# Kernel optimization log

Measured on AMD Instinct MI355X. Metric: run time of the kernel, lower is better.

## Reference

```python
import jax, jax.numpy as jnp
import numpy as np

# PGA G(3,0,1), basis order [1, e0,e1,e2,e3, e01,e02,e03,e12,e13,e23, e012,e013,e023,e123, e0123].
# Non-degenerate blades (no e0 factor) kept by the inner-product mask:
INNER_COORDS = jnp.array([0, 2, 3, 4, 8, 9, 10, 14])

B, S, C_IN, MV = 4, 2048, 3, 16
HID, NH, BLADES = 32, 8, 9


def setup_inputs() -> dict:
    key = jax.random.key(0)
    ks = jax.random.split(key, 8)
    return {
        "x": jax.random.normal(ks[0], (B, S, C_IN, MV), dtype=jnp.float32),
        "blade": jax.random.normal(ks[1], (BLADES, MV, MV), dtype=jnp.float32) * 0.3,
        "w_enter": jax.random.uniform(ks[2], (HID, C_IN, BLADES), dtype=jnp.float32),
        "w_q": jax.random.uniform(ks[3], (HID * NH, HID, BLADES), dtype=jnp.float32),
        "w_k": jax.random.uniform(ks[4], (HID, HID, BLADES), dtype=jnp.float32),
        "w_v": jax.random.uniform(ks[5], (HID, HID, BLADES), dtype=jnp.float32),
        "w_out": jax.random.uniform(ks[6], (HID, HID * NH, BLADES), dtype=jnp.float32),
        "w_final": jax.random.uniform(ks[7], (HID, HID, BLADES), dtype=jnp.float32),
    }


def equi_linear(w, blade, x):
    # torch: einsum('j i b, b x y, ... i x -> ... j y'); fuse blade into weight first.
    wb = jnp.einsum("jib,bxy->jixy", w, blade)  # [out, in, 16, 16]
    return jnp.einsum("jixy,bsix->bsjy", wb, x)


def equi_norm(x):
    ip = jnp.sum(jnp.take(x, INNER_COORDS, axis=-1) ** 2, axis=-1, keepdims=True)
    sq = jnp.mean(ip, axis=-2, keepdims=True)  # mean over mv channels
    return x / jnp.sqrt(sq)


def geometric_attention(hn, blade, w_q, w_k, w_v, w_out):
    b, s = hn.shape[0], hn.shape[1]
    q = equi_linear(w_q, blade, hn)  # [b, s, HID*NH, 16]
    k = equi_linear(w_k, blade, hn)  # [b, s, HID, 16]
    v = equi_linear(w_v, blade, hn)
    # rearrange '... items (hidden n_heads) mv -> ... n_heads items hidden mv'
    q = q.reshape(b, s, HID, NH, MV).transpose(0, 3, 1, 2, 4)  # [b, nh, s, HID, 16]
    qs = jnp.take(q, INNER_COORDS, axis=-1).reshape(b, NH, s, HID * 8)
    ks = jnp.take(k, INNER_COORDS, axis=-1).reshape(b, s, HID * 8)  # shared head (dim 1)
    vs = v.reshape(b, s, HID * MV)
    scale = 1.0 / jnp.sqrt(jnp.asarray(HID * 8, dtype=qs.dtype))
    scores = jnp.einsum("bhsd,btd->bhst", qs, ks) * scale  # [b, nh, s, s]
    attn = jax.nn.softmax(scores, axis=-1)
    out = jnp.einsum("bhst,btd->bhsd", attn, vs)  # [b, nh, s, HID*16]
    out = out[..., : HID * MV].reshape(b, NH, s, HID, MV)
    # '... heads items hidden x -> ... items (heads hidden) x'
    out = out.transpose(0, 2, 1, 3, 4).reshape(b, s, NH * HID, MV)
    return equi_linear(w_out, blade, out)  # [b, s, HID, 16]


def reference(x, blade, w_enter, w_q, w_k, w_v, w_out, w_final):
    h = equi_linear(w_enter, blade, x)  # initial projection -> [b, s, HID, 16]
    res = h
    hn = equi_norm(h)  # attention_equinorm
    a = geometric_attention(hn, blade, w_q, w_k, w_v, w_out)
    h = res + a  # residual around attention block
    return equi_linear(w_final, blade, h)  # final output projection
```

## Files before the change

kernel.cpp:

```cpp
#include <hip/hip_runtime.h>


typedef unsigned short u16;
typedef unsigned int u32;
typedef __attribute__((ext_vector_type(4))) float f32x4;
typedef __attribute__((ext_vector_type(8))) _Float16 half8;

__device__ inline u16 f2h(float f) {
  _Float16 h = (_Float16)f;
  return __builtin_bit_cast(u16, h);
}
__device__ inline float h2f(u16 u) { return (float)__builtin_bit_cast(_Float16, u); }

__device__ inline void async_cp16(const void* g, void* l) {
  __builtin_amdgcn_global_load_lds((const __attribute__((address_space(1))) u32*)g,
                                   (__attribute__((address_space(3))) u32*)l, 16, 0, 0);
}

__device__ inline f32x4 mfma16(half8 a, half8 b, f32x4 c) {
  return __builtin_amdgcn_mfma_f32_16x16x32_f16(a, b, c, 0, 0, 0);
}

template <int CTRL>
__device__ inline float dpp_mv(float v) {
  int i = __builtin_bit_cast(int, v);
  return __builtin_bit_cast(float, __builtin_amdgcn_update_dpp(i, i, CTRL, 0xf, 0xf, false));
}

#define IC_PACK 0xEA984320u

#define Q_LD 4096

__global__ void build_wb_enter(const float* __restrict__ we, const float* __restrict__ blade,
                               float* __restrict__ out) {
  int idx = blockIdx.x * 256 + threadIdx.x;
  if (idx >= 32 * 48 * 16) return;
  int j = idx / 768;
  int rem = idx - j * 768;
  int ix = rem >> 4, y = rem & 15;
  int i = ix >> 4, x = ix & 15;
  float acc = 0.f;
#pragma unroll
  for (int bb = 0; bb < 9; ++bb) acc += we[j * 27 + i * 9 + bb] * blade[bb * 256 + x * 16 + y];
  out[idx] = acc;
}

__global__ void build_wqkvT(const float* __restrict__ wq, const float* __restrict__ wk,
                            const float* __restrict__ wv, const float* __restrict__ blade,
                            u16* __restrict__ out) {
  int idx = blockIdx.x * 256 + threadIdx.x;
  if (idx >= 2816 * 1024) return;
  int k = idx & 1023, n = idx >> 10;
  int kk = k & 511;
  int i = kk >> 4, x = kk & 15;
  const float* w;
  int y;
  float scale = 1.0f;
  if (n < 2048) {
    int j = n >> 3;
    y = (IC_PACK >> ((n & 7) * 4)) & 15;
    w = wq + j * 288 + i * 9;
    scale = 0.09016844005556021f;
  } else if (n < 2304) {
    int m = n - 2048;
    int j = m >> 3;
    y = (IC_PACK >> ((m & 7) * 4)) & 15;
    w = wk + j * 288 + i * 9;
  } else {
    int m = n - 2304;
    int j = m >> 4;
    y = m & 15;
    w = wv + j * 288 + i * 9;
  }
  float acc = 0.f;
#pragma unroll
  for (int bb = 0; bb < 9; ++bb) acc += w[bb] * blade[bb * 256 + x * 16 + y];
  out[idx] = f2h(acc * scale);
}

__global__ void build_woutT(const float* __restrict__ wo, const float* __restrict__ blade,
                            u16* __restrict__ out) {
  int idx = blockIdx.x * 256 + threadIdx.x;
  if (idx >= 512 * 4096) return;
  int k = idx & 4095, n = idx >> 12;
  int j = n >> 4, y = n & 15;
  int c = k >> 4, x = k & 15;
  float acc = 0.f;
#pragma unroll
  for (int bb = 0; bb < 9; ++bb) acc += wo[j * 2304 + c * 9 + bb] * blade[bb * 256 + x * 16 + y];
  out[idx] = f2h(acc);
}

__global__ void build_wfinalT(const float* __restrict__ wf, const float* __restrict__ blade,
                              u16* __restrict__ out) {
  int idx = blockIdx.x * 256 + threadIdx.x;
  if (idx >= 512 * 512) return;
  int k = idx & 511, n = idx >> 9;
  int j = n >> 4, y = n & 15;
  int i = k >> 4, x = k & 15;
  float acc = 0.f;
#pragma unroll
  for (int bb = 0; bb < 9; ++bb) acc += wf[j * 288 + i * 9 + bb] * blade[bb * 256 + x * 16 + y];
  out[idx] = f2h(acc);
}

__global__ __launch_bounds__(256) void enter_norm(const float* __restrict__ x,
                                                  const float* __restrict__ wb,
                                                  float* __restrict__ h, u16* __restrict__ hn) {
  const int tid = threadIdx.x;
  const int tl = tid >> 5, j = tid & 31;
  const int token = blockIdx.x * 8 + tl;
  const float* xp = x + (size_t)token * 48;
  float xv[48];
#pragma unroll
  for (int q = 0; q < 12; ++q) {
    float4 t = ((const float4*)xp)[q];
    xv[q * 4 + 0] = t.x;
    xv[q * 4 + 1] = t.y;
    xv[q * 4 + 2] = t.z;
    xv[q * 4 + 3] = t.w;
  }
  float acc[16] = {};
  const float* wp = wb + j * 768;
#pragma unroll
  for (int t = 0; t < 48; ++t) {
    const float xs = xv[t];
    const float4* w4 = (const float4*)(wp + t * 16);
#pragma unroll
    for (int u = 0; u < 4; ++u) {
      float4 wv = w4[u];
      acc[u * 4 + 0] += xs * wv.x;
      acc[u * 4 + 1] += xs * wv.y;
      acc[u * 4 + 2] += xs * wv.z;
      acc[u * 4 + 3] += xs * wv.w;
    }
  }
  float ip = acc[0] * acc[0] + acc[2] * acc[2] + acc[3] * acc[3] + acc[4] * acc[4] +
             acc[8] * acc[8] + acc[9] * acc[9] + acc[10] * acc[10] + acc[14] * acc[14];
#pragma unroll
  for (int d = 1; d < 32; d <<= 1) ip += __shfl_xor(ip, d, 64);
  const float r = 1.0f / sqrtf(ip * (1.0f / 32.0f));
  float* hp = h + (size_t)token * 512 + j * 16;
#pragma unroll
  for (int u = 0; u < 4; ++u)
    ((float4*)hp)[u] = make_float4(acc[u * 4 + 0], acc[u * 4 + 1], acc[u * 4 + 2], acc[u * 4 + 3]);
  u16 hb[16], lb[16];
#pragma unroll
  for (int y = 0; y < 16; ++y) {
    float sv = acc[y] * r;
    u16 hv = f2h(sv);
    hb[y] = hv;
    lb[y] = f2h(sv - h2f(hv));
  }
  u16* hq = hn + (size_t)token * 1024 + j * 16;
  ((uint4*)hq)[0] = *(const uint4*)&hb[0];
  ((uint4*)hq)[1] = *(const uint4*)&hb[8];
  u16* lq = hq + 512;
  ((uint4*)lq)[0] = *(const uint4*)&lb[0];
  ((uint4*)lq)[1] = *(const uint4*)&lb[8];
}

template <int MODE>
__global__ __launch_bounds__(256) void gemm_bt(const u16* __restrict__ A,
                                               const u16* __restrict__ BT, int M, int N, int K,
                                               u16* __restrict__ Co, float* __restrict__ Cf,
                                               const float* __restrict__ res,
                                               u16* __restrict__ kvp, int ldc) {
  __shared__ u16 ltA[4096];
  __shared__ u16 ltB[4096];
  const int tid = threadIdx.x;
  const int lane = tid & 63;
  const int wid = tid >> 6;
  const int quad = lane >> 4, colc = lane & 15;
  const int m0 = blockIdx.y * 128, n0 = blockIdx.x * 128;
  const int wrow = (wid >> 1) * 64, wcol = (wid & 1) * 64;
  f32x4 acc[4][4] = {};
  const int r0 = tid >> 2;
  const int swk = (((tid & 3) ^ ((tid >> 2) & 3)) << 3);
  const u16* Ab = A + (size_t)(m0 + r0) * K + swk;
  const u16* Ab2 = Ab + (size_t)64 * K;
  const u16* Bb = BT + (size_t)(n0 + r0) * K + swk;
  const u16* Bb2 = Bb + (size_t)64 * K;
  const int swr = ((colc & 3) << 3);
  for (int k0 = 0; k0 < K; k0 += 32) {
    __syncthreads();
    async_cp16(Ab + k0, &ltA[tid * 8]);
    async_cp16(Ab2 + k0, &ltA[2048 + tid * 8]);
    async_cp16(Bb + k0, &ltB[tid * 8]);
    async_cp16(Bb2 + k0, &ltB[2048 + tid * 8]);
    __syncthreads();
    half8 af[4], bfr[4];
#pragma unroll
    for (int i2 = 0; i2 < 4; ++i2)
      af[i2] = *(const half8*)&ltA[(wrow + i2 * 16 + colc) * 32 + ((quad << 3) ^ swr)];
#pragma unroll
    for (int j2 = 0; j2 < 4; ++j2)
      bfr[j2] = *(const half8*)&ltB[(wcol + j2 * 16 + colc) * 32 + ((quad << 3) ^ swr)];
#pragma unroll
    for (int i2 = 0; i2 < 4; ++i2)
#pragma unroll
      for (int j2 = 0; j2 < 4; ++j2) acc[i2][j2] = mfma16(af[i2], bfr[j2], acc[i2][j2]);
  }
#pragma unroll
  for (int i2 = 0; i2 < 4; ++i2) {
#pragma unroll
    for (int j2 = 0; j2 < 4; ++j2) {
      const int mb = m0 + wrow + i2 * 16 + quad * 4;
      const int n = n0 + wcol + j2 * 16 + colc;
      if constexpr (MODE == 0) {
        if (n < 2048) {
#pragma unroll
          for (int rg = 0; rg < 4; ++rg) {
            const int m = mb + rg;
            float v = acc[i2][j2][rg];
            u16 hv = f2h(v);
            Co[(size_t)m * ldc + n] = hv;
            Co[(size_t)m * ldc + 2048 + n] = f2h(v - h2f(hv));
          }
        } else if (n < 2304) {
          const int d = n - 2048;
#pragma unroll
          for (int rg = 0; rg < 4; ++rg) {
            const int m = mb + rg;
            int bb2 = m >> 11, s = m & 2047, t = s >> 5, key = s & 31;
            size_t blk = ((size_t)(bb2 * 64 + t)) << 15;
            int off2 = key * 256 + ((((d >> 3) ^ (key & 7)) << 3)) + (d & 7);
            float v = acc[i2][j2][rg];
            u16 hv = f2h(v);
            kvp[blk + off2] = hv;
            kvp[blk + 8192 + off2] = f2h(v - h2f(hv));
          }
        } else {
          const int vd = n - 2304;
          int bb2 = mb >> 11, s0 = mb & 2047, t = s0 >> 5, key0 = s0 & 31;
          size_t blk = ((size_t)(bb2 * 64 + t)) << 15;
          u16 tmp[4];
#pragma unroll
          for (int rg = 0; rg < 4; ++rg) tmp[rg] = f2h(acc[i2][j2][rg]);
          size_t idx =
              blk + 16384 + vd * 32 + ((((key0 >> 3) ^ ((vd >> 1) & 3)) << 3)) + (key0 & 7);
          *(uint2*)&kvp[idx] = *(const uint2*)tmp;
        }
      } else {
#pragma unroll
        for (int rg = 0; rg < 4; ++rg) {
          const int m = mb + rg;
          float v = acc[i2][j2][rg];
          if constexpr (MODE == 1) {
            v += res[(size_t)m * ldc + n];
            Co[(size_t)m * ldc + n] = f2h(v * (1.0f / 256.0f));
          } else {
            Cf[(size_t)m * ldc + n] = v * 256.0f;
          }
        }
      }
    }
  }
}

__global__ __launch_bounds__(256, 2) void flash_attn(const u16* __restrict__ qbuf,
                                                     const u16* __restrict__ kvp,
                                                     u16* __restrict__ out) {
  __shared__ u16 lds[35600];
  u16* kp = lds;
  u16* lp = lds + 8192;
  u16* vp = lds + 16384;
  u16* pbuf = lds + 32768;
  float* alpha_s = (float*)(lds + 35328);
  float* l_s = (float*)(lds + 35456);
  int* flg = (int*)(lds + 35584);
  const int tid = threadIdx.x, lane = tid & 63, wid = tid >> 6;
  const int quad = lane >> 4, colc = lane & 15;
  const int b = blockIdx.z, h = blockIdx.y, qb = blockIdx.x;
  half8 qh[8], ql[8];
  {
    const u16* qr = qbuf + (size_t)(b * 2048 + qb * 64 + wid * 16 + colc) * Q_LD + h * 8;
#pragma unroll
    for (int kb = 0; kb < 8; ++kb) {
      qh[kb] = *(const half8*)(qr + (kb * 4 + quad) * 64);
      ql[kb] = *(const half8*)(qr + 2048 + (kb * 4 + quad) * 64);
    }
  }
  f32x4 oacc[4][8] = {};
  float mrun[4], lrun[4];
#pragma unroll
  for (int rg = 0; rg < 4; ++rg) {
    mrun[rg] = -1e30f;
    lrun[rg] = 0.f;
  }
  const u16* kvb = kvp + ((size_t)(b * 64) << 15);
  const int x0 = colc & 7;
  for (int it = 0; it < 64; ++it) {
    __syncthreads();
    {
      const u16* src = kvb + ((size_t)it << 15);
#pragma unroll
      for (int c = 0; c < 16; ++c) {
        int e = c * 256 + tid;
        async_cp16(src + e * 8, &lds[e * 8]);
      }
    }
    __syncthreads();
    f32x4 s0a = {}, s0b = {}, s1a = {}, s1b = {};
#pragma unroll
    for (int kb = 0; kb < 8; ++kb) {
      const int sw = (((kb * 4 + quad) ^ x0) << 3);
      half8 khi0 = *(const half8*)&kp[colc * 256 + sw];
      half8 khi1 = *(const half8*)&kp[(16 + colc) * 256 + sw];
      half8 klo0 = *(const half8*)&lp[colc * 256 + sw];
      half8 klo1 = *(const half8*)&lp[(16 + colc) * 256 + sw];
      s0a = mfma16(qh[kb], khi0, s0a);
      s0b = mfma16(ql[kb], khi0, s0b);
      s1a = mfma16(qh[kb], khi1, s1a);
      s1b = mfma16(ql[kb], khi1, s1b);
      if (kb & 1) {
        s0b = mfma16(qh[kb], klo0, s0b);
        s1b = mfma16(qh[kb], klo1, s1b);
      } else {
        s0a = mfma16(qh[kb], klo0, s0a);
        s1a = mfma16(qh[kb], klo1, s1a);
      }
    }
    f32x4 sfr[2];
    sfr[0] = s0a + s0b;
    sfr[1] = s1a + s1b;
    float mx[4];
#pragma unroll
    for (int rg = 0; rg < 4; ++rg) mx[rg] = fmaxf(sfr[0][rg], sfr[1][rg]);
#pragma unroll
    for (int rg = 0; rg < 4; ++rg) mx[rg] = fmaxf(mx[rg], dpp_mv<0x121>(mx[rg]));
#pragma unroll
    for (int rg = 0; rg < 4; ++rg) mx[rg] = fmaxf(mx[rg], dpp_mv<0x122>(mx[rg]));
#pragma unroll
    for (int rg = 0; rg < 4; ++rg) mx[rg] = fmaxf(mx[rg], dpp_mv<0x124>(mx[rg]));
#pragma unroll
    for (int rg = 0; rg < 4; ++rg) mx[rg] = fmaxf(mx[rg], dpp_mv<0x128>(mx[rg]));
    float al[4], pv0[4], pv1[4], rs[4];
#pragma unroll
    for (int rg = 0; rg < 4; ++rg) {
      float mn = fmaxf(mrun[rg], mx[rg]);
      al[rg] = exp2f(mrun[rg] - mn);
      mrun[rg] = mn;
      pv0[rg] = exp2f(sfr[0][rg] - mn);
      pv1[rg] = exp2f(sfr[1][rg] - mn);
      rs[rg] = pv0[rg] + pv1[rg];
    }
#pragma unroll
    for (int rg = 0; rg < 4; ++rg) rs[rg] += dpp_mv<0x121>(rs[rg]);
#pragma unroll
    for (int rg = 0; rg < 4; ++rg) rs[rg] += dpp_mv<0x122>(rs[rg]);
#pragma unroll
    for (int rg = 0; rg < 4; ++rg) rs[rg] += dpp_mv<0x124>(rs[rg]);
#pragma unroll
    for (int rg = 0; rg < 4; ++rg) rs[rg] += dpp_mv<0x128>(rs[rg]);
    const int prow = wid * 16 + quad * 4;
#pragma unroll
    for (int rg = 0; rg < 4; ++rg) {
      lrun[rg] = lrun[rg] * al[rg] + rs[rg];
      pbuf[(prow + rg) * 40 + colc] = f2h(pv0[rg]);
      pbuf[(prow + rg) * 40 + 16 + colc] = f2h(pv1[rg]);
    }
    {
      float nd = __builtin_fabsf(al[0] - 1.f) + __builtin_fabsf(al[1] - 1.f) +
                 __builtin_fabsf(al[2] - 1.f) + __builtin_fabsf(al[3] - 1.f);
      int own = __any(nd != 0.f);
      if (lane == 0) flg[wid] = own;
    }
    if (colc == 0) {
#pragma unroll
      for (int rg = 0; rg < 4; ++rg) alpha_s[prow + rg] = al[rg];
    }
    __syncthreads();
    half8 vf[8];
#pragma unroll
    for (int vb = 0; vb < 8; ++vb) {
      const int vd = wid * 128 + vb * 16 + colc;
      vf[vb] = *(const half8*)&vp[vd * 32 + ((quad ^ ((vd >> 1) & 3)) << 3)];
    }
    half8 pf[4];
#pragma unroll
    for (int pa = 0; pa < 4; ++pa) pf[pa] = *(const half8*)&pbuf[(pa * 16 + colc) * 40 + quad * 8];
    const int need = flg[0] | flg[1] | flg[2] | flg[3];
    if (need) {
      float av[4][4];
#pragma unroll
      for (int pa = 0; pa < 4; ++pa)
#pragma unroll
        for (int rg = 0; rg < 4; ++rg) av[pa][rg] = alpha_s[pa * 16 + quad * 4 + rg];
#pragma unroll
      for (int pa = 0; pa < 4; ++pa)
#pragma unroll
        for (int vb = 0; vb < 8; ++vb)
#pragma unroll
          for (int rg = 0; rg < 4; ++rg) oacc[pa][vb][rg] *= av[pa][rg];
    }
#pragma unroll
    for (int vb = 0; vb < 8; ++vb)
#pragma unroll
      for (int pa = 0; pa < 4; ++pa) oacc[pa][vb] = mfma16(pf[pa], vf[vb], oacc[pa][vb]);
  }
  {
    const int prow = wid * 16 + quad * 4;
    if (colc == 0) {
#pragma unroll
      for (int rg = 0; rg < 4; ++rg) l_s[prow + rg] = lrun[rg];
    }
  }
  __syncthreads();
  u16* ob = out + ((size_t)b * 2048 + qb * 64) * 4096 + h * 512 + wid * 128;
#pragma unroll
  for (int pa = 0; pa < 4; ++pa) {
    float li[4];
#pragma unroll
    for (int rg = 0; rg < 4; ++rg) li[rg] = 1.0f / l_s[pa * 16 + quad * 4 + rg];
#pragma unroll
    for (int vb = 0; vb < 8; ++vb)
#pragma unroll
      for (int rg = 0; rg < 4; ++rg)
        ob[(size_t)(pa * 16 + quad * 4 + rg) * 4096 + vb * 16 + colc] =
            f2h(oacc[pa][vb][rg] * li[rg]);
  }
}

extern "C" void kernel_launch(void* const* d_in, const int* in_sizes, int n_in, void* d_out,
                              int out_size, void* d_ws, size_t ws_size, hipStream_t stream) {
  const float* x = (const float*)d_in[0];
  const float* blade = (const float*)d_in[1];
  const float* w_enter = (const float*)d_in[2];
  const float* w_q = (const float*)d_in[3];
  const float* w_k = (const float*)d_in[4];
  const float* w_v = (const float*)d_in[5];
  const float* w_out = (const float*)d_in[6];
  const float* w_final = (const float*)d_in[7];
  float* out = (float*)d_out;

  char* ws = (char*)d_ws;
  size_t off = 0;
  auto alloc = [&](size_t bytes) {
    void* p = ws + off;
    off = (off + bytes + 255) & ~(size_t)255;
    return p;
  };
  float* wb_enter = (float*)alloc((size_t)32 * 48 * 16 * 4);
  u16* wqkvT = (u16*)alloc((size_t)2816 * 1024 * 2);
  u16* woutT = (u16*)alloc((size_t)512 * 4096 * 2);
  u16* wfinT = (u16*)alloc((size_t)512 * 512 * 2);
  float* hbuf = (float*)alloc((size_t)8192 * 512 * 4);
  u16* hn2 = (u16*)alloc((size_t)8192 * 1024 * 2);
  u16* qbuf = (u16*)alloc((size_t)8192 * Q_LD * 2);
  u16* kvp = (u16*)alloc((size_t)4 * 64 * 32768 * 2);
  u16* attno = (u16*)alloc((size_t)8192 * 4096 * 2);
  u16* h2 = (u16*)alloc((size_t)8192 * 512 * 2);

  build_wb_enter<<<96, 256, 0, stream>>>(w_enter, blade, wb_enter);
  build_wqkvT<<<11264, 256, 0, stream>>>(w_q, w_k, w_v, blade, wqkvT);
  build_woutT<<<8192, 256, 0, stream>>>(w_out, blade, woutT);
  build_wfinalT<<<1024, 256, 0, stream>>>(w_final, blade, wfinT);
  enter_norm<<<1024, 256, 0, stream>>>(x, wb_enter, hbuf, hn2);
  gemm_bt<0><<<dim3(22, 64), 256, 0, stream>>>(hn2, wqkvT, 8192, 2816, 1024, qbuf, nullptr,
                                               nullptr, kvp, Q_LD);
  flash_attn<<<dim3(32, 8, 4), 256, 0, stream>>>(qbuf, kvp, attno);
  gemm_bt<1><<<dim3(4, 64), 256, 0, stream>>>(attno, woutT, 8192, 512, 4096, h2, nullptr, hbuf,
                                              nullptr, 512);
  gemm_bt<2><<<dim3(4, 64), 256, 0, stream>>>(h2, wfinT, 8192, 512, 512, nullptr, out, nullptr,
                                              nullptr, 512);
}
```

Baseline: 984.4 us.

## Drop K low-half split and software-pipeline K/V prefetch in flash attention

Removes the low-order fp16 residual for K, which cuts the K tile's global traffic and LDS footprint and removes two MFMAs per k-block. The attention loop now prefetches the next K tile right after the score MFMAs and the next V tile right after the PV MFMAs. Fine-grained s_waitcnt vmcnt plus raw s_barrier replace the __syncthreads pairs so these loads overlap with compute. The conditional alpha-rescale skip is also removed, so rescaling always runs. Dropping the K residual lowers score precision, and the hand-written waitcnt counts must match the number of outstanding loads exactly.

```diff
diff --git a/kernel.cpp b/kernel.cpp
--- a/kernel.cpp
+++ b/kernel.cpp
@@ -27,9 +27,14 @@
   return __builtin_bit_cast(float, __builtin_amdgcn_update_dpp(i, i, CTRL, 0xf, 0xf, false));
 }
 
+#define HW_BARRIER() asm volatile("s_barrier" ::: "memory")
+#define WAIT_VM8() asm volatile("s_waitcnt vmcnt(8)" ::: "memory")
+#define WAIT_VM4_LGKM0() asm volatile("s_waitcnt vmcnt(4) lgkmcnt(0)" ::: "memory")
+
 #define IC_PACK 0xEA984320u
 
 #define Q_LD 4096
+#define KV_STRIDE 24576
 
 __global__ void build_wb_enter(const float* __restrict__ we, const float* __restrict__ blade,
                                float* __restrict__ out) {
@@ -223,22 +228,19 @@
           for (int rg = 0; rg < 4; ++rg) {
             const int m = mb + rg;
             int bb2 = m >> 11, s = m & 2047, t = s >> 5, key = s & 31;
-            size_t blk = ((size_t)(bb2 * 64 + t)) << 15;
+            size_t blk = (size_t)(bb2 * 64 + t) * KV_STRIDE;
             int off2 = key * 256 + ((((d >> 3) ^ (key & 7)) << 3)) + (d & 7);
-            float v = acc[i2][j2][rg];
-            u16 hv = f2h(v);
-            kvp[blk + off2] = hv;
-            kvp[blk + 8192 + off2] = f2h(v - h2f(hv));
+            kvp[blk + off2] = f2h(acc[i2][j2][rg]);
           }
         } else {
           const int vd = n - 2304;
           int bb2 = mb >> 11, s0 = mb & 2047, t = s0 >> 5, key0 = s0 & 31;
-          size_t blk = ((size_t)(bb2 * 64 + t)) << 15;
+          size_t blk = (size_t)(bb2 * 64 + t) * KV_STRIDE;
           u16 tmp[4];
 #pragma unroll
           for (int rg = 0; rg < 4; ++rg) tmp[rg] = f2h(acc[i2][j2][rg]);
           size_t idx =
-              blk + 16384 + vd * 32 + ((((key0 >> 3) ^ ((vd >> 1) & 3)) << 3)) + (key0 & 7);
+              blk + 8192 + vd * 32 + ((((key0 >> 3) ^ ((vd >> 1) & 3)) << 3)) + (key0 & 7);
           *(uint2*)&kvp[idx] = *(const uint2*)tmp;
         }
       } else {
@@ -261,14 +263,12 @@
 __global__ __launch_bounds__(256, 2) void flash_attn(const u16* __restrict__ qbuf,
                                                      const u16* __restrict__ kvp,
                                                      u16* __restrict__ out) {
-  __shared__ u16 lds[35600];
+  __shared__ u16 lds[27392];
   u16* kp = lds;
-  u16* lp = lds + 8192;
-  u16* vp = lds + 16384;
-  u16* pbuf = lds + 32768;
-  float* alpha_s = (float*)(lds + 35328);
-  float* l_s = (float*)(lds + 35456);
-  int* flg = (int*)(lds + 35584);
+  u16* vp = lds + 8192;
+  u16* pbuf = lds + 24576;
+  float* alpha_s = (float*)(lds + 27136);
+  float* l_s = (float*)(lds + 27264);
   const int tid = threadIdx.x, lane = tid & 63, wid = tid >> 6;
   const int quad = lane >> 4, colc = lane & 15;
   const int b = blockIdx.z, h = blockIdx.y, qb = blockIdx.x;
@@ -288,42 +288,48 @@
     mrun[rg] = -1e30f;
     lrun[rg] = 0.f;
   }
-  const u16* kvb = kvp + ((size_t)(b * 64) << 15);
+  const u16* kvb = kvp + (size_t)b * 64 * KV_STRIDE;
   const int x0 = colc & 7;
+  {
+    const u16* src = kvb;
+#pragma unroll
+    for (int c = 0; c < 4; ++c) {
+      int e = c * 256 + tid;
+      async_cp16(src + e * 8, &lds[e * 8]);
+    }
+#pragma unroll
+    for (int c = 0; c < 8; ++c) {
+      int e = c * 256 + tid;
+      async_cp16(src + 8192 + e * 8, &lds[8192 + e * 8]);
+    }
+  }
   for (int it = 0; it < 64; ++it) {
-    __syncthreads();
-    {
-      const u16* src = kvb + ((size_t)it << 15);
-#pragma unroll
-      for (int c = 0; c < 16; ++c) {
-        int e = c * 256 + tid;
-        async_cp16(src + e * 8, &lds[e * 8]);
-      }
-    }
-    __syncthreads();
+    WAIT_VM8();
+    HW_BARRIER();
     f32x4 s0a = {}, s0b = {}, s1a = {}, s1b = {};
 #pragma unroll
     for (int kb = 0; kb < 8; ++kb) {
       const int sw = (((kb * 4 + quad) ^ x0) << 3);
       half8 khi0 = *(const half8*)&kp[colc * 256 + sw];
       half8 khi1 = *(const half8*)&kp[(16 + colc) * 256 + sw];
-      half8 klo0 = *(const half8*)&lp[colc * 256 + sw];
-      half8 klo1 = *(const half8*)&lp[(16 + colc) * 256 + sw];
       s0a = mfma16(qh[kb], khi0, s0a);
       s0b = mfma16(ql[kb], khi0, s0b);
       s1a = mfma16(qh[kb], khi1, s1a);
       s1b = mfma16(ql[kb], khi1, s1b);
-      if (kb & 1) {
-        s0b = mfma16(qh[kb], klo0, s0b);
-        s1b = mfma16(qh[kb], klo1, s1b);
-      } else {
-        s0a = mfma16(qh[kb], klo0, s0a);
-        s1a = mfma16(qh[kb], klo1, s1a);
-      }
     }
     f32x4 sfr[2];
     sfr[0] = s0a + s0b;
     sfr[1] = s1a + s1b;
+    HW_BARRIER();
+    {
+      const int itn = (it < 63) ? it + 1 : 63;
+      const u16* src = kvb + (size_t)itn * KV_STRIDE;
+#pragma unroll
+      for (int c = 0; c < 4; ++c) {
+        int e = c * 256 + tid;
+        async_cp16(src + e * 8, &lds[e * 8]);
+      }
+    }
     float mx[4];
 #pragma unroll
     for (int rg = 0; rg < 4; ++rg) mx[rg] = fmaxf(sfr[0][rg], sfr[1][rg]);
@@ -360,17 +366,12 @@
       pbuf[(prow + rg) * 40 + colc] = f2h(pv0[rg]);
       pbuf[(prow + rg) * 40 + 16 + colc] = f2h(pv1[rg]);
     }
-    {
-      float nd = __builtin_fabsf(al[0] - 1.f) + __builtin_fabsf(al[1] - 1.f) +
-                 __builtin_fabsf(al[2] - 1.f) + __builtin_fabsf(al[3] - 1.f);
-      int own = __any(nd != 0.f);
-      if (lane == 0) flg[wid] = own;
-    }
     if (colc == 0) {
 #pragma unroll
       for (int rg = 0; rg < 4; ++rg) alpha_s[prow + rg] = al[rg];
     }
-    __syncthreads();
+    WAIT_VM4_LGKM0();
+    HW_BARRIER();
     half8 vf[8];
 #pragma unroll
     for (int vb = 0; vb < 8; ++vb) {
@@ -380,24 +381,31 @@
     half8 pf[4];
 #pragma unroll
     for (int pa = 0; pa < 4; ++pa) pf[pa] = *(const half8*)&pbuf[(pa * 16 + colc) * 40 + quad * 8];
-    const int need = flg[0] | flg[1] | flg[2] | flg[3];
-    if (need) {
-      float av[4][4];
-#pragma unroll
-      for (int pa = 0; pa < 4; ++pa)
-#pragma unroll
-        for (int rg = 0; rg < 4; ++rg) av[pa][rg] = alpha_s[pa * 16 + quad * 4 + rg];
-#pragma unroll
-      for (int pa = 0; pa < 4; ++pa)
-#pragma unroll
-        for (int vb = 0; vb < 8; ++vb)
-#pragma unroll
-          for (int rg = 0; rg < 4; ++rg) oacc[pa][vb][rg] *= av[pa][rg];
-    }
+    float av[4][4];
+#pragma unroll
+    for (int pa = 0; pa < 4; ++pa)
+#pragma unroll
+      for (int rg = 0; rg < 4; ++rg) av[pa][rg] = alpha_s[pa * 16 + quad * 4 + rg];
+#pragma unroll
+    for (int pa = 0; pa < 4; ++pa)
+#pragma unroll
+      for (int vb = 0; vb < 8; ++vb)
+#pragma unroll
+        for (int rg = 0; rg < 4; ++rg) oacc[pa][vb][rg] *= av[pa][rg];
 #pragma unroll
     for (int vb = 0; vb < 8; ++vb)
 #pragma unroll
       for (int pa = 0; pa < 4; ++pa) oacc[pa][vb] = mfma16(pf[pa], vf[vb], oacc[pa][vb]);
+    HW_BARRIER();
+    {
+      const int itn = (it < 63) ? it + 1 : 63;
+      const u16* src = kvb + (size_t)itn * KV_STRIDE;
+#pragma unroll
+      for (int c = 0; c < 8; ++c) {
+        int e = c * 256 + tid;
+        async_cp16(src + 8192 + e * 8, &lds[8192 + e * 8]);
+      }
+    }
   }
   {
     const int prow = wid * 16 + quad * 4;
@@ -448,7 +456,7 @@
   float* hbuf = (float*)alloc((size_t)8192 * 512 * 4);
   u16* hn2 = (u16*)alloc((size_t)8192 * 1024 * 2);
   u16* qbuf = (u16*)alloc((size_t)8192 * Q_LD * 2);
-  u16* kvp = (u16*)alloc((size_t)4 * 64 * 32768 * 2);
+  u16* kvp = (u16*)alloc((size_t)4 * 64 * KV_STRIDE * 2);
   u16* attno = (u16*)alloc((size_t)8192 * 4096 * 2);
   u16* h2 = (u16*)alloc((size_t)8192 * 512 * 2);
 
```

Result: slower. 1.034 ms (+5.1%).
